# Optimization experiments

Hardware: AMD Instinct MI355X
Metric: run time of the kernel (lower is better)

## Reference

```python
import jax, jax.numpy as jnp
import numpy as np

N_NODES = 100000
IN_DIM = 512
OUT_DIM = 512  # output_dim(128) * head_num(4)
N_EDGES = 1600000
EDGE_DIM = 16
N_GRAPHS = 16
EPS = 1e-5
NEG_SLOPE = 0.2  # LeakyReLU(negative_slope=0.2) from loss_type='RELU'


def setup_inputs() -> dict:
    key = jax.random.key(0)
    k1, k2, k3, k4, k5, k6 = jax.random.split(key, 6)
    x = jax.random.normal(k1, (N_NODES, IN_DIM), dtype=jnp.float32)
    edge_attr = jax.random.normal(k2, (N_EDGES, EDGE_DIM), dtype=jnp.float32)
    edge_index = jax.random.randint(k3, (2, N_EDGES), 0, N_NODES, dtype=jnp.int64)
    batch = jnp.sort(jax.random.randint(k4, (N_NODES,), 0, N_GRAPHS, dtype=jnp.int64))
    # Linear(input_dim, output_dim*head_num) params
    W = jax.random.normal(k5, (OUT_DIM, IN_DIM), dtype=jnp.float32) / np.sqrt(IN_DIM)
    b = jax.random.normal(k6, (OUT_DIM,), dtype=jnp.float32) * 0.01
    # LayerNorm affine params
    gamma = jnp.ones((OUT_DIM,), dtype=jnp.float32)
    beta = jnp.zeros((OUT_DIM,), dtype=jnp.float32)
    return {"x": x, "edge_attr": edge_attr, "edge_index": edge_index,
            "batch": batch, "W": W, "b": b, "gamma": gamma, "beta": beta}


def reference(x, edge_attr, edge_index, batch, W, b, gamma, beta):
    # Eval mode: node/edge dropout and output Dropout are identity.
    # Linear: [N, IN_DIM] @ [IN_DIM, OUT_DIM] + b
    x_before = jnp.einsum('ni,oi->no', x, W) + b
    # Per-segment LayerNorm with norm_type='layer' reduces to rowwise LayerNorm:
    # each row of each segment is normalized over the feature dim independently,
    # and segments are contiguous (batch sorted) so concat order is unchanged.
    mean = jnp.mean(x_before, axis=-1, keepdims=True)
    var = jnp.mean(jnp.square(x_before - mean), axis=-1, keepdims=True)
    normed = (x_before - mean) * jax.lax.rsqrt(var + EPS) * gamma + beta
    # LeakyReLU(0.2)
    return jnp.where(normed >= 0, normed, NEG_SLOPE * normed)
```

## Files before the change

### kernel.cpp

```cpp
#include <hip/hip_runtime.h>
#include <hip/hip_bf16.h>

#define M_NODES 100000
#define KDIM    512
#define NDIM    512
#define MT      64
#define BK      32
#define EPS     1e-5f
#define SLOPE   0.2f

typedef __attribute__((ext_vector_type(8))) short bf16x8;
typedef __attribute__((ext_vector_type(4))) float f32x4;
typedef __attribute__((ext_vector_type(4))) int   i32x4;

#define LDS_A    0
#define LDS_B    4096
#define LDS_RED  36864
#define LDS_SIZE 38912

__device__ __forceinline__ unsigned short f2bf(float x) {
    unsigned u = __float_as_uint(x);
    u += 0x7FFFu + ((u >> 16) & 1u);
    return (unsigned short)(u >> 16);
}

template<bool F32>
__device__ __forceinline__ i32x4 load8(const char* p) {
    if constexpr (!F32) {
        return *(const i32x4*)p;
    } else {
        f32x4 a = *(const f32x4*)p;
        f32x4 b = *(const f32x4*)(p + 16);
        union { unsigned short s[8]; i32x4 v; } u;
        u.s[0]=f2bf(a[0]); u.s[1]=f2bf(a[1]); u.s[2]=f2bf(a[2]); u.s[3]=f2bf(a[3]);
        u.s[4]=f2bf(b[0]); u.s[5]=f2bf(b[1]); u.s[6]=f2bf(b[2]); u.s[7]=f2bf(b[3]);
        return u.v;
    }
}

template<bool F32>
__device__ __forceinline__ float ldp(const void* p, int i) {
    if constexpr (F32) return ((const float*)p)[i];
    else return __bfloat162float(((const __hip_bfloat16*)p)[i]);
}

template<bool F32>
__global__ __launch_bounds__(512, 2)
void fused_gemm_ln_lrelu(const void* __restrict__ Xv, const void* __restrict__ Wv,
                         const void* __restrict__ Bv, const void* __restrict__ Gv,
                         const void* __restrict__ Pv, void* __restrict__ Ov)
{
    {
        const unsigned* Xw = (const unsigned*)Xv;
        int l = threadIdx.x & 63;
        float f0 = __uint_as_float(Xw[l]);
        float f1 = __uint_as_float(Xw[l + 64]);
        int cnt = __popcll(__ballot(fabsf(f0) < 64.0f))
                + __popcll(__ballot(fabsf(f1) < 64.0f));
        bool is_f32 = (cnt >= 96);
        if (is_f32 != F32) return;
    }

    constexpr int ES = F32 ? 4 : 2;
    __shared__ __align__(16) char smem[LDS_SIZE];

    const int tid  = threadIdx.x;
    const int wave = tid >> 6;
    const int lane = tid & 63;
    const int quad = lane >> 4;
    const int lcol = lane & 15;
    const int wrow = wave >> 2;
    const int wcol = wave & 3;
    const int mbase = blockIdx.x * MT;

    const int pos = quad ^ (lcol & 3) ^ ((lcol >> 2) & 3);
    const unsigned offA = (unsigned)(LDS_A + (wrow * 32 + lcol) * 64 + pos * 16);
    const unsigned offB = (unsigned)(LDS_B + (wcol * 128 + lcol) * 64 + pos * 16);

    const int prow = tid >> 2;
    const int ppc  = tid & 3;
    const int wp   = ppc ^ (prow & 3) ^ ((prow >> 2) & 3);
    const unsigned offWB = (unsigned)(LDS_B + prow * 64 + wp * 16);
    const unsigned offWA = (unsigned)(LDS_A + prow * 64 + wp * 16);
    int ag = mbase + prow; if (ag > M_NODES - 1) ag = M_NODES - 1;
    const char* aG = (const char*)Xv + ((size_t)ag * KDIM + ppc * 8) * ES;
    const char* bG = (const char*)Wv + ((size_t)prow * KDIM + ppc * 8) * ES;

    f32x4 acc[2][8];
#pragma unroll
    for (int mt = 0; mt < 2; ++mt)
#pragma unroll
        for (int nt = 0; nt < 8; ++nt)
            acc[mt][nt] = (f32x4){0.f, 0.f, 0.f, 0.f};

    i32x4 pa; i32x4 pb[4];
    if (tid < 256) pa = load8<F32>(aG);
#pragma unroll
    for (int i = 0; i < 4; ++i)
        pb[i] = load8<F32>(bG + (size_t)i * (128 * KDIM * ES));

    for (int kk = 0; kk < KDIM; kk += BK) {
        __syncthreads();
        if (tid < 256) *(i32x4*)(smem + offWA) = pa;
#pragma unroll
        for (int i = 0; i < 4; ++i)
            *(i32x4*)(smem + offWB + i * 8192) = pb[i];
        __syncthreads();

        if (kk + BK < KDIM) {
            const int kb = (kk + BK) * ES;
            if (tid < 256) pa = load8<F32>(aG + kb);
#pragma unroll
            for (int i = 0; i < 4; ++i)
                pb[i] = load8<F32>(bG + (size_t)i * (128 * KDIM * ES) + kb);
        }

        bf16x8 a0 = *(const bf16x8*)(smem + offA);
        bf16x8 a1 = *(const bf16x8*)(smem + offA + 1024);
#pragma unroll
        for (int nt = 0; nt < 8; ++nt) {
            bf16x8 b = *(const bf16x8*)(smem + offB + nt * 1024);
            acc[0][nt] = __builtin_amdgcn_mfma_f32_16x16x32_bf16(a0, b, acc[0][nt], 0, 0, 0);
            acc[1][nt] = __builtin_amdgcn_mfma_f32_16x16x32_bf16(a1, b, acc[1][nt], 0, 0, 0);
        }
    }

    float sum_[2][4] = {{0,0,0,0},{0,0,0,0}};
    float ssq_[2][4] = {{0,0,0,0},{0,0,0,0}};
#pragma unroll
    for (int nt = 0; nt < 8; ++nt) {
        int col = wcol * 128 + nt * 16 + lcol;
        float bv = ldp<F32>(Bv, col);
#pragma unroll
        for (int mt = 0; mt < 2; ++mt)
#pragma unroll
            for (int r = 0; r < 4; ++r) {
                float v = acc[mt][nt][r] + bv;
                acc[mt][nt][r] = v;
                sum_[mt][r] += v;
                ssq_[mt][r] = fmaf(v, v, ssq_[mt][r]);
            }
    }
#pragma unroll
    for (int off = 1; off < 16; off <<= 1) {
#pragma unroll
        for (int mt = 0; mt < 2; ++mt)
#pragma unroll
            for (int r = 0; r < 4; ++r) {
                sum_[mt][r] += __shfl_xor(sum_[mt][r], off, 64);
                ssq_[mt][r] += __shfl_xor(ssq_[mt][r], off, 64);
            }
    }
    float* red = (float*)(smem + LDS_RED);
    if (lcol == 0) {
#pragma unroll
        for (int mt = 0; mt < 2; ++mt)
#pragma unroll
            for (int r = 0; r < 4; ++r) {
                int brow = wrow * 32 + mt * 16 + quad * 4 + r;
                red[brow * 8 + wcol * 2 + 0] = sum_[mt][r];
                red[brow * 8 + wcol * 2 + 1] = ssq_[mt][r];
            }
    }
    __syncthreads();

    float mean_[2][4], rs_[2][4];
#pragma unroll
    for (int mt = 0; mt < 2; ++mt)
#pragma unroll
        for (int r = 0; r < 4; ++r) {
            int brow = wrow * 32 + mt * 16 + quad * 4 + r;
            float S = red[brow*8+0] + red[brow*8+2] + red[brow*8+4] + red[brow*8+6];
            float Q = red[brow*8+1] + red[brow*8+3] + red[brow*8+5] + red[brow*8+7];
            float m = S * (1.0f / NDIM);
            float var = Q * (1.0f / NDIM) - m * m;
            mean_[mt][r] = m;
            rs_[mt][r] = rsqrtf(var + EPS);
        }

    if constexpr (!F32) {
        unsigned short* so = (unsigned short*)(smem + LDS_B);
#pragma unroll
        for (int h = 0; h < 2; ++h) {
            __syncthreads();
            if (wrow == h) {
#pragma unroll
                for (int nt = 0; nt < 8; ++nt) {
                    int col = wcol * 128 + nt * 16 + lcol;
                    float g  = ldp<F32>(Gv, col);
                    float be = ldp<F32>(Pv, col);
#pragma unroll
                    for (int mt = 0; mt < 2; ++mt)
#pragma unroll
                        for (int r = 0; r < 4; ++r) {
                            int lrow = mt * 16 + quad * 4 + r;
                            float v = (acc[mt][nt][r] - mean_[mt][r]) * rs_[mt][r] * g + be;
                            v = (v >= 0.f) ? v : SLOPE * v;
                            so[lrow * 512 + col] = f2bf(v);
                        }
                }
            }
            __syncthreads();
#pragma unroll
            for (int i = 0; i < 4; ++i) {
                int lrow = i * 8 + wave;
                int grow = mbase + h * 32 + lrow;
                if (grow < M_NODES) {
                    i32x4 v = *(const i32x4*)(so + lrow * 512 + lane * 8);
                    *(i32x4*)((char*)Ov + (size_t)grow * (NDIM*2) + lane * 16) = v;
                }
            }
        }
    } else {
        float* sof = (float*)(smem + LDS_B);
#pragma unroll
        for (int p = 0; p < 4; ++p) {
            __syncthreads();
            if (wrow == (p >> 1)) {
                const int mt = p & 1;
#pragma unroll
                for (int nt = 0; nt < 8; ++nt) {
                    int col = wcol * 128 + nt * 16 + lcol;
                    float g  = ldp<F32>(Gv, col);
                    float be = ldp<F32>(Pv, col);
#pragma unroll
                    for (int r = 0; r < 4; ++r) {
                        float v = (acc[mt][nt][r] - mean_[mt][r]) * rs_[mt][r] * g + be;
                        v = (v >= 0.f) ? v : SLOPE * v;
                        sof[(quad * 4 + r) * 512 + col] = v;
                    }
                }
            }
            __syncthreads();
#pragma unroll
            for (int i = 0; i < 4; ++i) {
                int chunk = i * 8 + wave;
                int row = chunk >> 1, half = chunk & 1;
                int grow = mbase + p * 16 + row;
                if (grow < M_NODES) {
                    i32x4 v = *(const i32x4*)((char*)sof + row * 2048 + half * 1024 + lane * 16);
                    *(i32x4*)((char*)Ov + (size_t)grow * (NDIM*4) + half * 1024 + lane * 16) = v;
                }
            }
        }
    }
}

extern "C" void kernel_launch(void* const* d_in, const int* in_sizes, int n_in,
                              void* d_out, int out_size, void* d_ws, size_t ws_size,
                              hipStream_t stream) {
    const void* X = d_in[0];
    const void* W = d_in[4];
    const void* B = d_in[5];
    const void* G = d_in[6];
    const void* P = d_in[7];

    int grid = (M_NODES + MT - 1) / MT;
    fused_gemm_ln_lrelu<false><<<grid, 512, 0, stream>>>(X, W, B, G, P, d_out);
    fused_gemm_ln_lrelu<true ><<<grid, 512, 0, stream>>>(X, W, B, G, P, d_out);
}
```

Measured before the change: 542.0 us.

## Pre-swizzle W to bf16 and double-buffer LDS with direct global-to-LDS loads

A new prep kernel converts W to bf16 and writes it to workspace in a pre-swizzled per-slab layout. The main GEMM then copies B tiles straight into LDS with global_load_lds and double-buffers both the A and B tiles. A register prefetch of A runs three slabs ahead, and the loop drops from two barriers per slab to one. Output staging rows are padded to cut LDS bank conflicts, and launch bounds move to 4. This should hide load latency and remove the per-block fp32-to-bf16 conversion of W, at the cost of doubled LDS (~74KB), which may limit occupancy, plus an extra small kernel launch.

```diff
diff --git a/kernel.cpp b/kernel.cpp
--- a/kernel.cpp
+++ b/kernel.cpp
@@ -6,17 +6,23 @@
 #define NDIM    512
 #define MT      64
 #define BK      32
+#define NSLAB   16
 #define EPS     1e-5f
 #define SLOPE   0.2f
 
 typedef __attribute__((ext_vector_type(8))) short bf16x8;
 typedef __attribute__((ext_vector_type(4))) float f32x4;
 typedef __attribute__((ext_vector_type(4))) int   i32x4;
-
-#define LDS_A    0
-#define LDS_B    4096
-#define LDS_RED  36864
-#define LDS_SIZE 38912
+typedef __attribute__((ext_vector_type(2))) unsigned u32x2;
+
+#define LDS_A0   0
+#define LDS_A1   4096
+#define LDS_B0   8192
+#define LDS_B1   40960
+#define LDS_RED  73728
+#define LDS_SIZE 75776
+
+__device__ __forceinline__ int swz(int r) { return (r & 3) ^ ((r >> 2) & 3); }
 
 __device__ __forceinline__ unsigned short f2bf(float x) {
     unsigned u = __float_as_uint(x);
@@ -44,22 +50,44 @@
     else return __bfloat162float(((const __hip_bfloat16*)p)[i]);
 }
 
+__device__ __forceinline__ bool gate_is_f32(const void* Xv) {
+    const unsigned* Xw = (const unsigned*)Xv;
+    int l = threadIdx.x & 63;
+    float f0 = __uint_as_float(Xw[l]);
+    float f1 = __uint_as_float(Xw[l + 64]);
+    int cnt = __popcll(__ballot(fabsf(f0) < 64.0f))
+            + __popcll(__ballot(fabsf(f1) < 64.0f));
+    return cnt >= 96;
+}
+
+__device__ __forceinline__ void gload16(const void* g, void* l) {
+    __builtin_amdgcn_global_load_lds(
+        (const __attribute__((address_space(1))) unsigned*)g,
+        (__attribute__((address_space(3))) unsigned*)l, 16, 0, 0);
+}
+
 template<bool F32>
-__global__ __launch_bounds__(512, 2)
-void fused_gemm_ln_lrelu(const void* __restrict__ Xv, const void* __restrict__ Wv,
+__global__ __launch_bounds__(512, 1)
+void prep_w(const void* __restrict__ Xv, const void* __restrict__ Wv,
+            void* __restrict__ ws)
+{
+    if (gate_is_f32(Xv) != F32) return;
+    constexpr int ES = F32 ? 4 : 2;
+    int idx = blockIdx.x * 512 + threadIdx.x;
+    int p = idx & 3;
+    int r = (idx >> 2) & 511;
+    int s = idx >> 11;
+    i32x4 v = load8<F32>((const char*)Wv + ((size_t)r * KDIM + s * BK + p * 8) * ES);
+    *(i32x4*)((char*)ws + (size_t)s * 32768 + r * 64 + (p ^ swz(r)) * 16) = v;
+}
+
+template<bool F32>
+__global__ __launch_bounds__(512, 4)
+void fused_gemm_ln_lrelu(const void* __restrict__ Xv, const void* __restrict__ WSv,
                          const void* __restrict__ Bv, const void* __restrict__ Gv,
                          const void* __restrict__ Pv, void* __restrict__ Ov)
 {
-    {
-        const unsigned* Xw = (const unsigned*)Xv;
-        int l = threadIdx.x & 63;
-        float f0 = __uint_as_float(Xw[l]);
-        float f1 = __uint_as_float(Xw[l + 64]);
-        int cnt = __popcll(__ballot(fabsf(f0) < 64.0f))
-                + __popcll(__ballot(fabsf(f1) < 64.0f));
-        bool is_f32 = (cnt >= 96);
-        if (is_f32 != F32) return;
-    }
+    if (gate_is_f32(Xv) != F32) return;
 
     constexpr int ES = F32 ? 4 : 2;
     __shared__ __align__(16) char smem[LDS_SIZE];
@@ -73,18 +101,39 @@
     const int wcol = wave & 3;
     const int mbase = blockIdx.x * MT;
 
-    const int pos = quad ^ (lcol & 3) ^ ((lcol >> 2) & 3);
-    const unsigned offA = (unsigned)(LDS_A + (wrow * 32 + lcol) * 64 + pos * 16);
-    const unsigned offB = (unsigned)(LDS_B + (wcol * 128 + lcol) * 64 + pos * 16);
-
-    const int prow = tid >> 2;
-    const int ppc  = tid & 3;
-    const int wp   = ppc ^ (prow & 3) ^ ((prow >> 2) & 3);
-    const unsigned offWB = (unsigned)(LDS_B + prow * 64 + wp * 16);
-    const unsigned offWA = (unsigned)(LDS_A + prow * 64 + wp * 16);
-    int ag = mbase + prow; if (ag > M_NODES - 1) ag = M_NODES - 1;
-    const char* aG = (const char*)Xv + ((size_t)ag * KDIM + ppc * 8) * ES;
-    const char* bG = (const char*)Wv + ((size_t)prow * KDIM + ppc * 8) * ES;
+    const int pos = quad ^ swz(lcol);
+    const unsigned offA = (unsigned)((wrow * 32 + lcol) * 64 + pos * 16);
+    const unsigned offB = (unsigned)((wcol * 128 + lcol) * 64 + pos * 16);
+
+    const int ar = tid >> 3, ap = (tid & 7) >> 1, ah = tid & 1;
+    int ag = mbase + ar; if (ag > M_NODES - 1) ag = M_NODES - 1;
+    const char* aG = (const char*)Xv + ((size_t)ag * KDIM + ap * 8 + ah * 4) * ES;
+    const unsigned offWA = (unsigned)(ar * 64 + (ap ^ swz(ar)) * 16 + ah * 8);
+
+    const char* bG  = (const char*)WSv + (size_t)wave * 4096 + (size_t)lane * 16;
+    const unsigned bdst = (unsigned)(wave * 4096);
+
+    f32x4 aRf[3]; u32x2 aRb[3];
+    auto loada = [&](int s, int slot) {
+        if constexpr (F32) aRf[slot] = *(const f32x4*)(aG + (size_t)s * (BK * 4));
+        else               aRb[slot] = *(const u32x2*)(aG + (size_t)s * (BK * 2));
+    };
+    auto awrite = [&](unsigned abuf, int slot) {
+        u32x2 w;
+        if constexpr (F32) {
+            f32x4 v = aRf[slot];
+            w[0] = (unsigned)f2bf(v[0]) | ((unsigned)f2bf(v[1]) << 16);
+            w[1] = (unsigned)f2bf(v[2]) | ((unsigned)f2bf(v[3]) << 16);
+        } else {
+            w = aRb[slot];
+        }
+        *(u32x2*)(smem + abuf + offWA) = w;
+    };
+    auto stageB = [&](const char* src, unsigned bbuf) {
+#pragma unroll
+        for (int i = 0; i < 4; ++i)
+            gload16(src + i * 1024, smem + bbuf + bdst + i * 1024);
+    };
 
     f32x4 acc[2][8];
 #pragma unroll
@@ -93,35 +142,46 @@
         for (int nt = 0; nt < 8; ++nt)
             acc[mt][nt] = (f32x4){0.f, 0.f, 0.f, 0.f};
 
-    i32x4 pa; i32x4 pb[4];
-    if (tid < 256) pa = load8<F32>(aG);
-#pragma unroll
-    for (int i = 0; i < 4; ++i)
-        pb[i] = load8<F32>(bG + (size_t)i * (128 * KDIM * ES));
-
-    for (int kk = 0; kk < KDIM; kk += BK) {
-        __syncthreads();
-        if (tid < 256) *(i32x4*)(smem + offWA) = pa;
-#pragma unroll
-        for (int i = 0; i < 4; ++i)
-            *(i32x4*)(smem + offWB + i * 8192) = pb[i];
-        __syncthreads();
-
-        if (kk + BK < KDIM) {
-            const int kb = (kk + BK) * ES;
-            if (tid < 256) pa = load8<F32>(aG + kb);
-#pragma unroll
-            for (int i = 0; i < 4; ++i)
-                pb[i] = load8<F32>(bG + (size_t)i * (128 * KDIM * ES) + kb);
-        }
-
-        bf16x8 a0 = *(const bf16x8*)(smem + offA);
-        bf16x8 a1 = *(const bf16x8*)(smem + offA + 1024);
+    const char* bGs = bG;
+    stageB(bGs, LDS_B0); bGs += 32768;
+    loada(0, 0); loada(1, 1); loada(2, 2);
+    awrite(LDS_A0, 0);
+    asm volatile("s_waitcnt lgkmcnt(0)" ::: "memory");
+    __builtin_amdgcn_s_barrier();
+    __builtin_amdgcn_sched_barrier(0);
+
+#pragma unroll
+    for (int t = 0; t < NSLAB; ++t) {
+        const unsigned Acur = (t & 1) ? LDS_A1 : LDS_A0;
+        const unsigned Bcur = (t & 1) ? LDS_B1 : LDS_B0;
+        const unsigned Anx  = (t & 1) ? LDS_A0 : LDS_A1;
+        const unsigned Bnx  = (t & 1) ? LDS_B0 : LDS_B1;
+
+        if (t + 1 < NSLAB) {
+            stageB(bGs, Bnx); bGs += 32768;
+            __builtin_amdgcn_sched_barrier(0);
+            awrite(Anx, (t + 1) % 3);
+            if (t + 3 < NSLAB) loada(t + 3, t % 3);
+            __builtin_amdgcn_sched_barrier(0);
+        }
+
+        bf16x8 a0 = *(const bf16x8*)(smem + Acur + offA);
+        bf16x8 a1 = *(const bf16x8*)(smem + Acur + offA + 1024);
 #pragma unroll
         for (int nt = 0; nt < 8; ++nt) {
-            bf16x8 b = *(const bf16x8*)(smem + offB + nt * 1024);
+            bf16x8 b = *(const bf16x8*)(smem + Bcur + offB + nt * 1024);
             acc[0][nt] = __builtin_amdgcn_mfma_f32_16x16x32_bf16(a0, b, acc[0][nt], 0, 0, 0);
             acc[1][nt] = __builtin_amdgcn_mfma_f32_16x16x32_bf16(a1, b, acc[1][nt], 0, 0, 0);
+        }
+
+        if (t + 1 < NSLAB) {
+            asm volatile("s_waitcnt lgkmcnt(0)" ::: "memory");
+            if (t + 3 < NSLAB)
+                asm volatile("s_waitcnt vmcnt(1)" ::: "memory");
+            else
+                asm volatile("s_waitcnt vmcnt(0)" ::: "memory");
+            __builtin_amdgcn_s_barrier();
+            __builtin_amdgcn_sched_barrier(0);
         }
     }
 
@@ -179,7 +239,7 @@
         }
 
     if constexpr (!F32) {
-        unsigned short* so = (unsigned short*)(smem + LDS_B);
+        unsigned short* so = (unsigned short*)(smem + LDS_B0);
 #pragma unroll
         for (int h = 0; h < 2; ++h) {
             __syncthreads();
@@ -196,7 +256,7 @@
                             int lrow = mt * 16 + quad * 4 + r;
                             float v = (acc[mt][nt][r] - mean_[mt][r]) * rs_[mt][r] * g + be;
                             v = (v >= 0.f) ? v : SLOPE * v;
-                            so[lrow * 512 + col] = f2bf(v);
+                            so[lrow * 520 + col] = f2bf(v);
                         }
                 }
             }
@@ -206,13 +266,13 @@
                 int lrow = i * 8 + wave;
                 int grow = mbase + h * 32 + lrow;
                 if (grow < M_NODES) {
-                    i32x4 v = *(const i32x4*)(so + lrow * 512 + lane * 8);
+                    i32x4 v = *(const i32x4*)(so + lrow * 520 + lane * 8);
                     *(i32x4*)((char*)Ov + (size_t)grow * (NDIM*2) + lane * 16) = v;
                 }
             }
         }
     } else {
-        float* sof = (float*)(smem + LDS_B);
+        float* sof = (float*)(smem + LDS_B0);
 #pragma unroll
         for (int p = 0; p < 4; ++p) {
             __syncthreads();
@@ -227,7 +287,7 @@
                     for (int r = 0; r < 4; ++r) {
                         float v = (acc[mt][nt][r] - mean_[mt][r]) * rs_[mt][r] * g + be;
                         v = (v >= 0.f) ? v : SLOPE * v;
-                        sof[(quad * 4 + r) * 512 + col] = v;
+                        sof[(quad * 4 + r) * 516 + col] = v;
                     }
                 }
             }
@@ -238,7 +298,7 @@
                 int row = chunk >> 1, half = chunk & 1;
                 int grow = mbase + p * 16 + row;
                 if (grow < M_NODES) {
-                    i32x4 v = *(const i32x4*)((char*)sof + row * 2048 + half * 1024 + lane * 16);
+                    i32x4 v = *(const i32x4*)((char*)sof + row * 2064 + half * 1024 + lane * 16);
                     *(i32x4*)((char*)Ov + (size_t)grow * (NDIM*4) + half * 1024 + lane * 16) = v;
                 }
             }
@@ -255,7 +315,10 @@
     const void* G = d_in[6];
     const void* P = d_in[7];
 
+    prep_w<false><<<64, 512, 0, stream>>>(X, W, d_ws);
+    prep_w<true ><<<64, 512, 0, stream>>>(X, W, d_ws);
+
     int grid = (M_NODES + MT - 1) / MT;
-    fused_gemm_ln_lrelu<false><<<grid, 512, 0, stream>>>(X, W, B, G, P, d_out);
-    fused_gemm_ln_lrelu<true ><<<grid, 512, 0, stream>>>(X, W, B, G, P, d_out);
-}
+    fused_gemm_ln_lrelu<false><<<grid, 512, 0, stream>>>(X, d_ws, B, G, P, d_out);
+    fused_gemm_ln_lrelu<true ><<<grid, 512, 0, stream>>>(X, d_ws, B, G, P, d_out);
+}
```

After: 448.6 us. 17.2% less time.

## Prepack W into MFMA fragment order and stream operands from registers without LDS

Applied to the files above, without the earlier changes.

Adds a prep kernel that converts W to bf16 and reorders it into the per-lane MFMA fragment layout in the workspace. The main kernel then loads A and B fragments straight from global memory into registers, double or triple buffered, instead of staging them through LDS with two barriers per K step. Tile height drops to 32 rows with 256 threads and occupancy 3, and the output staging uses padded LDS rows to avoid bank conflicts. Each block now re-reads all of W from L2 and there is an extra launch, but the per-iteration LDS traffic and syncs go away.

```diff
diff --git a/kernel.cpp b/kernel.cpp
--- a/kernel.cpp
+++ b/kernel.cpp
@@ -4,8 +4,10 @@
 #define M_NODES 100000
 #define KDIM    512
 #define NDIM    512
-#define MT      64
+#define MT      32
 #define BK      32
+#define NSLAB   16
+#define NHALF   32
 #define EPS     1e-5f
 #define SLOPE   0.2f
 
@@ -13,10 +15,9 @@
 typedef __attribute__((ext_vector_type(4))) float f32x4;
 typedef __attribute__((ext_vector_type(4))) int   i32x4;
 
-#define LDS_A    0
-#define LDS_B    4096
-#define LDS_RED  36864
-#define LDS_SIZE 38912
+#define LDS_STG  0
+#define LDS_RED  33792
+#define LDS_SIZE 34816
 
 __device__ __forceinline__ unsigned short f2bf(float x) {
     unsigned u = __float_as_uint(x);
@@ -25,13 +26,13 @@
 }
 
 template<bool F32>
-__device__ __forceinline__ i32x4 load8(const char* p) {
+__device__ __forceinline__ bf16x8 load8(const char* p) {
     if constexpr (!F32) {
-        return *(const i32x4*)p;
+        return *(const bf16x8*)p;
     } else {
         f32x4 a = *(const f32x4*)p;
         f32x4 b = *(const f32x4*)(p + 16);
-        union { unsigned short s[8]; i32x4 v; } u;
+        union { unsigned short s[8]; bf16x8 v; } u;
         u.s[0]=f2bf(a[0]); u.s[1]=f2bf(a[1]); u.s[2]=f2bf(a[2]); u.s[3]=f2bf(a[3]);
         u.s[4]=f2bf(b[0]); u.s[5]=f2bf(b[1]); u.s[6]=f2bf(b[2]); u.s[7]=f2bf(b[3]);
         return u.v;
@@ -44,24 +45,43 @@
     else return __bfloat162float(((const __hip_bfloat16*)p)[i]);
 }
 
-template<bool F32>
-__global__ __launch_bounds__(512, 2)
-void fused_gemm_ln_lrelu(const void* __restrict__ Xv, const void* __restrict__ Wv,
+__device__ __forceinline__ bool gate_is_f32(const void* Xv) {
+    const unsigned* Xw = (const unsigned*)Xv;
+    int l = threadIdx.x & 63;
+    float f0 = __uint_as_float(Xw[l]);
+    float f1 = __uint_as_float(Xw[l + 64]);
+    int cnt = __popcll(__ballot(fabsf(f0) < 64.0f))
+            + __popcll(__ballot(fabsf(f1) < 64.0f));
+    return cnt >= 96;
+}
+
+template<bool F32>
+__global__ __launch_bounds__(512, 1)
+void prep_w(const void* __restrict__ Xv, const void* __restrict__ Wv,
+            void* __restrict__ ws)
+{
+    if (gate_is_f32(Xv) != F32) return;
+    constexpr int ES = F32 ? 4 : 2;
+    int idx = blockIdx.x * 512 + threadIdx.x;
+    int c = idx & 15;
+    int q = (idx >> 4) & 3;
+    int g = (idx >> 6) & 31;
+    int s = idx >> 11;
+    int n = g * 16 + c;
+    bf16x8 v = load8<F32>((const char*)Wv + ((size_t)n * KDIM + s * BK + q * 8) * ES);
+    *(bf16x8*)((char*)ws + (size_t)idx * 16) = v;
+}
+
+template<bool F32>
+__global__ __launch_bounds__(256, 3)
+void fused_gemm_ln_lrelu(const void* __restrict__ Xv, const void* __restrict__ WSv,
                          const void* __restrict__ Bv, const void* __restrict__ Gv,
                          const void* __restrict__ Pv, void* __restrict__ Ov)
 {
-    {
-        const unsigned* Xw = (const unsigned*)Xv;
-        int l = threadIdx.x & 63;
-        float f0 = __uint_as_float(Xw[l]);
-        float f1 = __uint_as_float(Xw[l + 64]);
-        int cnt = __popcll(__ballot(fabsf(f0) < 64.0f))
-                + __popcll(__ballot(fabsf(f1) < 64.0f));
-        bool is_f32 = (cnt >= 96);
-        if (is_f32 != F32) return;
-    }
-
-    constexpr int ES = F32 ? 4 : 2;
+    if (gate_is_f32(Xv) != F32) return;
+
+    constexpr int ES   = F32 ? 4 : 2;
+    constexpr int NBUF = F32 ? 2 : 3;
     __shared__ __align__(16) char smem[LDS_SIZE];
 
     const int tid  = threadIdx.x;
@@ -69,22 +89,46 @@
     const int lane = tid & 63;
     const int quad = lane >> 4;
     const int lcol = lane & 15;
-    const int wrow = wave >> 2;
-    const int wcol = wave & 3;
     const int mbase = blockIdx.x * MT;
 
-    const int pos = quad ^ (lcol & 3) ^ ((lcol >> 2) & 3);
-    const unsigned offA = (unsigned)(LDS_A + (wrow * 32 + lcol) * 64 + pos * 16);
-    const unsigned offB = (unsigned)(LDS_B + (wcol * 128 + lcol) * 64 + pos * 16);
-
-    const int prow = tid >> 2;
-    const int ppc  = tid & 3;
-    const int wp   = ppc ^ (prow & 3) ^ ((prow >> 2) & 3);
-    const unsigned offWB = (unsigned)(LDS_B + prow * 64 + wp * 16);
-    const unsigned offWA = (unsigned)(LDS_A + prow * 64 + wp * 16);
-    int ag = mbase + prow; if (ag > M_NODES - 1) ag = M_NODES - 1;
-    const char* aG = (const char*)Xv + ((size_t)ag * KDIM + ppc * 8) * ES;
-    const char* bG = (const char*)Wv + ((size_t)prow * KDIM + ppc * 8) * ES;
+    const char* aP0 = (const char*)Xv + ((size_t)(mbase + lcol) * KDIM + quad * 8) * ES;
+    const char* aP1 = aP0 + (size_t)16 * KDIM * ES;
+    const char* bP  = (const char*)WSv + (size_t)wave * 8192 + (size_t)lane * 16;
+
+    bf16x8 rAb[2][2];
+    f32x4  rAf[2][2][2];
+    bf16x8 rB[NBUF][4];
+    bf16x8 aC[2];
+
+    auto issueA = [&](int buf, int s) {
+        const int ka = s * BK * ES;
+        if constexpr (F32) {
+            rAf[buf][0][0] = *(const f32x4*)(aP0 + ka);
+            rAf[buf][0][1] = *(const f32x4*)(aP0 + ka + 16);
+            rAf[buf][1][0] = *(const f32x4*)(aP1 + ka);
+            rAf[buf][1][1] = *(const f32x4*)(aP1 + ka + 16);
+        } else {
+            rAb[buf][0] = *(const bf16x8*)(aP0 + ka);
+            rAb[buf][1] = *(const bf16x8*)(aP1 + ka);
+        }
+    };
+    auto cvtA = [&](int buf, int mt) -> bf16x8 {
+        if constexpr (F32) {
+            f32x4 lo = rAf[buf][mt][0], hi = rAf[buf][mt][1];
+            union { unsigned short s[8]; bf16x8 v; } u;
+            u.s[0]=f2bf(lo[0]); u.s[1]=f2bf(lo[1]); u.s[2]=f2bf(lo[2]); u.s[3]=f2bf(lo[3]);
+            u.s[4]=f2bf(hi[0]); u.s[5]=f2bf(hi[1]); u.s[6]=f2bf(hi[2]); u.s[7]=f2bf(hi[3]);
+            return u.v;
+        } else {
+            return rAb[buf][mt];
+        }
+    };
+    auto issueB = [&](int slot, int hh) {
+        const char* p = bP + (size_t)(hh >> 1) * 32768 + (hh & 1) * 4096;
+#pragma unroll
+        for (int j = 0; j < 4; ++j)
+            rB[slot][j] = *(const bf16x8*)(p + j * 1024);
+    };
 
     f32x4 acc[2][8];
 #pragma unroll
@@ -93,43 +137,32 @@
         for (int nt = 0; nt < 8; ++nt)
             acc[mt][nt] = (f32x4){0.f, 0.f, 0.f, 0.f};
 
-    i32x4 pa; i32x4 pb[4];
-    if (tid < 256) pa = load8<F32>(aG);
-#pragma unroll
-    for (int i = 0; i < 4; ++i)
-        pb[i] = load8<F32>(bG + (size_t)i * (128 * KDIM * ES));
-
-    for (int kk = 0; kk < KDIM; kk += BK) {
-        __syncthreads();
-        if (tid < 256) *(i32x4*)(smem + offWA) = pa;
-#pragma unroll
-        for (int i = 0; i < 4; ++i)
-            *(i32x4*)(smem + offWB + i * 8192) = pb[i];
-        __syncthreads();
-
-        if (kk + BK < KDIM) {
-            const int kb = (kk + BK) * ES;
-            if (tid < 256) pa = load8<F32>(aG + kb);
-#pragma unroll
-            for (int i = 0; i < 4; ++i)
-                pb[i] = load8<F32>(bG + (size_t)i * (128 * KDIM * ES) + kb);
-        }
-
-        bf16x8 a0 = *(const bf16x8*)(smem + offA);
-        bf16x8 a1 = *(const bf16x8*)(smem + offA + 1024);
-#pragma unroll
-        for (int nt = 0; nt < 8; ++nt) {
-            bf16x8 b = *(const bf16x8*)(smem + offB + nt * 1024);
-            acc[0][nt] = __builtin_amdgcn_mfma_f32_16x16x32_bf16(a0, b, acc[0][nt], 0, 0, 0);
-            acc[1][nt] = __builtin_amdgcn_mfma_f32_16x16x32_bf16(a1, b, acc[1][nt], 0, 0, 0);
-        }
+    issueA(0, 0); issueA(1, 1);
+    issueB(0, 0); issueB(1, 1);
+
+#pragma unroll
+    for (int h = 0; h < NHALF; ++h) {
+        const int s = h >> 1, half = h & 1;
+        if constexpr (NBUF == 3) { if (h + 2 < NHALF) issueB((h + 2) % 3, h + 2); }
+        if (half == 0) {
+            aC[0] = cvtA(s & 1, 0);
+            aC[1] = cvtA(s & 1, 1);
+            if (s + 2 < NSLAB) issueA(s & 1, s + 2);
+        }
+#pragma unroll
+        for (int j = 0; j < 4; ++j) {
+            bf16x8 b = rB[h % NBUF][j];
+            acc[0][half*4+j] = __builtin_amdgcn_mfma_f32_16x16x32_bf16(aC[0], b, acc[0][half*4+j], 0, 0, 0);
+            acc[1][half*4+j] = __builtin_amdgcn_mfma_f32_16x16x32_bf16(aC[1], b, acc[1][half*4+j], 0, 0, 0);
+        }
+        if constexpr (NBUF == 2) { if (h + 2 < NHALF) issueB(h % 2, h + 2); }
     }
 
     float sum_[2][4] = {{0,0,0,0},{0,0,0,0}};
     float ssq_[2][4] = {{0,0,0,0},{0,0,0,0}};
 #pragma unroll
     for (int nt = 0; nt < 8; ++nt) {
-        int col = wcol * 128 + nt * 16 + lcol;
+        int col = wave * 128 + nt * 16 + lcol;
         float bv = ldp<F32>(Bv, col);
 #pragma unroll
         for (int mt = 0; mt < 2; ++mt)
@@ -157,9 +190,9 @@
         for (int mt = 0; mt < 2; ++mt)
 #pragma unroll
             for (int r = 0; r < 4; ++r) {
-                int brow = wrow * 32 + mt * 16 + quad * 4 + r;
-                red[brow * 8 + wcol * 2 + 0] = sum_[mt][r];
-                red[brow * 8 + wcol * 2 + 1] = ssq_[mt][r];
+                int brow = mt * 16 + quad * 4 + r;
+                red[brow * 8 + wave * 2 + 0] = sum_[mt][r];
+                red[brow * 8 + wave * 2 + 1] = ssq_[mt][r];
             }
     }
     __syncthreads();
@@ -169,7 +202,7 @@
     for (int mt = 0; mt < 2; ++mt)
 #pragma unroll
         for (int r = 0; r < 4; ++r) {
-            int brow = wrow * 32 + mt * 16 + quad * 4 + r;
+            int brow = mt * 16 + quad * 4 + r;
             float S = red[brow*8+0] + red[brow*8+2] + red[brow*8+4] + red[brow*8+6];
             float Q = red[brow*8+1] + red[brow*8+3] + red[brow*8+5] + red[brow*8+7];
             float m = S * (1.0f / NDIM);
@@ -179,68 +212,55 @@
         }
 
     if constexpr (!F32) {
-        unsigned short* so = (unsigned short*)(smem + LDS_B);
-#pragma unroll
-        for (int h = 0; h < 2; ++h) {
+        unsigned short* so = (unsigned short*)(smem + LDS_STG);
+#pragma unroll
+        for (int nt = 0; nt < 8; ++nt) {
+            int col = wave * 128 + nt * 16 + lcol;
+            float g  = ldp<F32>(Gv, col);
+            float be = ldp<F32>(Pv, col);
+#pragma unroll
+            for (int mt = 0; mt < 2; ++mt)
+#pragma unroll
+                for (int r = 0; r < 4; ++r) {
+                    int lrow = mt * 16 + quad * 4 + r;
+                    float v = (acc[mt][nt][r] - mean_[mt][r]) * rs_[mt][r] * g + be;
+                    v = (v >= 0.f) ? v : SLOPE * v;
+                    so[lrow * 528 + col] = f2bf(v);
+                }
+        }
+        __syncthreads();
+#pragma unroll
+        for (int i = 0; i < 8; ++i) {
+            int lrow = i * 4 + wave;
+            int grow = mbase + lrow;
+            i32x4 v = *(const i32x4*)(so + lrow * 528 + lane * 8);
+            *(i32x4*)((char*)Ov + (size_t)grow * (NDIM*2) + lane * 16) = v;
+        }
+    } else {
+        float* sof = (float*)(smem + LDS_STG);
+#pragma unroll
+        for (int mt = 0; mt < 2; ++mt) {
+            if (mt) __syncthreads();
+#pragma unroll
+            for (int nt = 0; nt < 8; ++nt) {
+                int col = wave * 128 + nt * 16 + lcol;
+                float g  = ldp<F32>(Gv, col);
+                float be = ldp<F32>(Pv, col);
+#pragma unroll
+                for (int r = 0; r < 4; ++r) {
+                    float v = (acc[mt][nt][r] - mean_[mt][r]) * rs_[mt][r] * g + be;
+                    v = (v >= 0.f) ? v : SLOPE * v;
+                    sof[(quad * 4 + r) * 516 + col] = v;
+                }
+            }
             __syncthreads();
-            if (wrow == h) {
-#pragma unroll
-                for (int nt = 0; nt < 8; ++nt) {
-                    int col = wcol * 128 + nt * 16 + lcol;
-                    float g  = ldp<F32>(Gv, col);
-                    float be = ldp<F32>(Pv, col);
-#pragma unroll
-                    for (int mt = 0; mt < 2; ++mt)
-#pragma unroll
-                        for (int r = 0; r < 4; ++r) {
-                            int lrow = mt * 16 + quad * 4 + r;
-                            float v = (acc[mt][nt][r] - mean_[mt][r]) * rs_[mt][r] * g + be;
-                            v = (v >= 0.f) ? v : SLOPE * v;
-                            so[lrow * 512 + col] = f2bf(v);
-                        }
-                }
-            }
-            __syncthreads();
-#pragma unroll
-            for (int i = 0; i < 4; ++i) {
-                int lrow = i * 8 + wave;
-                int grow = mbase + h * 32 + lrow;
-                if (grow < M_NODES) {
-                    i32x4 v = *(const i32x4*)(so + lrow * 512 + lane * 8);
-                    *(i32x4*)((char*)Ov + (size_t)grow * (NDIM*2) + lane * 16) = v;
-                }
-            }
-        }
-    } else {
-        float* sof = (float*)(smem + LDS_B);
-#pragma unroll
-        for (int p = 0; p < 4; ++p) {
-            __syncthreads();
-            if (wrow == (p >> 1)) {
-                const int mt = p & 1;
-#pragma unroll
-                for (int nt = 0; nt < 8; ++nt) {
-                    int col = wcol * 128 + nt * 16 + lcol;
-                    float g  = ldp<F32>(Gv, col);
-                    float be = ldp<F32>(Pv, col);
-#pragma unroll
-                    for (int r = 0; r < 4; ++r) {
-                        float v = (acc[mt][nt][r] - mean_[mt][r]) * rs_[mt][r] * g + be;
-                        v = (v >= 0.f) ? v : SLOPE * v;
-                        sof[(quad * 4 + r) * 512 + col] = v;
-                    }
-                }
-            }
-            __syncthreads();
-#pragma unroll
-            for (int i = 0; i < 4; ++i) {
-                int chunk = i * 8 + wave;
+#pragma unroll
+            for (int i = 0; i < 8; ++i) {
+                int chunk = i * 4 + wave;
                 int row = chunk >> 1, half = chunk & 1;
-                int grow = mbase + p * 16 + row;
-                if (grow < M_NODES) {
-                    i32x4 v = *(const i32x4*)((char*)sof + row * 2048 + half * 1024 + lane * 16);
-                    *(i32x4*)((char*)Ov + (size_t)grow * (NDIM*4) + half * 1024 + lane * 16) = v;
-                }
+                int grow = mbase + mt * 16 + row;
+                i32x4 v = *(const i32x4*)((char*)sof + row * 2064 + half * 1024 + lane * 16);
+                *(i32x4*)((char*)Ov + (size_t)grow * (NDIM*4) + half * 1024 + lane * 16) = v;
             }
         }
     }
@@ -255,7 +275,10 @@
     const void* G = d_in[6];
     const void* P = d_in[7];
 
-    int grid = (M_NODES + MT - 1) / MT;
-    fused_gemm_ln_lrelu<false><<<grid, 512, 0, stream>>>(X, W, B, G, P, d_out);
-    fused_gemm_ln_lrelu<true ><<<grid, 512, 0, stream>>>(X, W, B, G, P, d_out);
-}
+    prep_w<false><<<64, 512, 0, stream>>>(X, W, d_ws);
+    prep_w<true ><<<64, 512, 0, stream>>>(X, W, d_ws);
+
+    int grid = M_NODES / MT;
+    fused_gemm_ln_lrelu<false><<<grid, 256, 0, stream>>>(X, d_ws, B, G, P, d_out);
+    fused_gemm_ln_lrelu<true ><<<grid, 256, 0, stream>>>(X, d_ws, B, G, P, d_out);
+}
```

After: 533.9 us. No clear change (-1.5%).
